# Kernel tuning notes

Hardware: AMD Instinct MI355X
Metric: run time of the kernel (lower is better)

Reference implementation:

```python
import jax, jax.numpy as jnp
import numpy as np

N, C, E, S = 16384, 128, 262144, 10
AVG_NUM_NEIGHBORS = 16.0
INV_SQRT3 = 1.0 / np.sqrt(3.0)


def setup_inputs() -> dict:
    key = jax.random.key(0)
    ks = jax.random.split(key, 15)
    return dict(
        node_specie=jax.random.randint(ks[0], (N,), 0, S),
        node_feats=jax.random.normal(ks[1], (N, C, 4), jnp.float32),   # irreps 0e+1o per channel
        edge_attrs=jax.random.normal(ks[2], (E, 4), jnp.float32),      # Y: 0e+1o
        edge_feats=jax.random.normal(ks[3], (E, 8), jnp.float32),      # radial scalars
        senders=jax.random.randint(ks[4], (E,), 0, N),
        receivers=jax.random.randint(ks[5], (E,), 0, N),
        W_sc0=jax.random.normal(ks[6], (S, C, C), jnp.float32),
        W_sc1=jax.random.normal(ks[7], (S, C, C), jnp.float32),
        W_pre0=jax.random.normal(ks[8], (C, C), jnp.float32),
        W_pre1=jax.random.normal(ks[9], (C, C), jnp.float32),
        W_mlp1=jax.random.normal(ks[10], (8, 64), jnp.float32),
        W_mlp2=jax.random.normal(ks[11], (64, 64), jnp.float32),
        W_mlp3=jax.random.normal(ks[12], (64, 4), jnp.float32),
        W_post0=jax.random.normal(ks[13], (C, 2, C), jnp.float32),
        W_post1=jax.random.normal(ks[14], (C, 2, C), jnp.float32),
    )


def reference(node_specie, node_feats, edge_attrs, edge_feats, senders, receivers,
              W_sc0, W_sc1, W_pre0, W_pre1, W_mlp1, W_mlp2, W_mlp3, W_post0, W_post1):
    inv_c = 1.0 / np.sqrt(C)
    s_in = node_feats[..., 0]      # [N,C] 0e
    v_in = node_feats[..., 1:4]    # [N,C,3] 1o

    # linear_sc: per-species equivariant linear (0e+1o -> hidden 0e+1o)
    sc_s = jnp.einsum('nc,ncd->nd', s_in, W_sc0[node_specie]) * inv_c
    sc_v = jnp.einsum('nci,ncd->ndi', v_in, W_sc1[node_specie]) * inv_c
    sc = jnp.concatenate([sc_s[..., None], sc_v], axis=-1)  # [N,C,4]

    # linear_premp: channel-mixing equivariant linear (same irreps)
    s = (s_in @ W_pre0) * inv_c                              # [N,C]
    v = jnp.einsum('nci,cd->ndi', v_in, W_pre1) * inv_c      # [N,C,3]

    # MessagePassingConvolution (channel axis kept instead of hk.vmap)
    se_s = s[senders]              # [E,C]
    se_v = v[senders]              # [E,C,3]
    a = edge_attrs[:, 1:4]         # drop 0e part of Y -> 1o
    dot = jnp.einsum('eci,ei->ec', se_v, a) * INV_SQRT3      # 1o x 1o -> 0e
    sva = se_s[..., None] * a[:, None, :]                    # 0e x 1o -> 1o

    # radial MLP -> one mixing scalar per irrep (num_irreps = 4), shared across channels
    h = jax.nn.silu((edge_feats @ W_mlp1) * (1.0 / np.sqrt(8.0)))
    h = jax.nn.silu((h @ W_mlp2) * 0.125)
    mix = (h @ W_mlp3) * 0.125                               # [E,4]

    # messages irreps 2x0e+2x1o: [s, dot | v, s*a], each block scaled by its mix scalar
    msg = jnp.concatenate([
        se_s[..., None] * mix[:, None, 0:1],
        dot[..., None] * mix[:, None, 1:2],
        se_v * mix[:, None, 2:3],
        sva * mix[:, None, 3:4],
    ], axis=-1)                                              # [E,C,8]

    agg = jnp.zeros((N, C, 8), msg.dtype).at[receivers].add(msg) / AVG_NUM_NEIGHBORS

    # linear_postmp: (2x0e+2x1o, C channels) -> (0e+1o, C channels)
    inv2c = 1.0 / np.sqrt(2 * C)
    o_s = jnp.einsum('ncm,cmd->nd', agg[..., :2], W_post0) * inv2c
    o_v = jnp.einsum('ncmi,cmd->ndi', agg[..., 2:].reshape(N, C, 2, 3), W_post1) * inv2c
    node_out = jnp.concatenate([o_s[..., None], o_v], axis=-1)  # [N,C,4]
    return node_out, sc
```

## Files before the change

### kernel.cpp

```cpp
#include <hip/hip_runtime.h>
#include <hip/hip_bf16.h>

#define N_NODES 16384
#define C_DIM   128
#define E_EDGES 262144
#define S_SPEC  10
#define CHUNK   256
#define GNODES  32
#define NSLICE  8
#define PROWS   16544
#define PTILES  1034

__device__ __constant__ const float INV_C  = 0.08838834764831845f;
__device__ __constant__ const float INV_2C = 0.0625f;
#define F_INV_SQRT3 0.5773502691896258f
#define F_INV_SQRT8 0.35355339059327373f
#define F_INV_AVG   0.0625f

typedef __attribute__((ext_vector_type(8))) short bf16x8;
typedef __attribute__((ext_vector_type(4))) float f32x4;

__device__ __forceinline__ float silu(float x) {
    return x / (1.0f + __expf(-x));
}

__device__ __forceinline__ unsigned short f2bf(float x) {
    __hip_bfloat16 h = __float2bfloat16(x);
    return *reinterpret_cast<unsigned short*>(&h);
}

__device__ __forceinline__ unsigned int pack2bf(float lo, float hi) {
    return (unsigned int)f2bf(lo) | ((unsigned int)f2bf(hi) << 16);
}

__device__ __forceinline__ float bf2f(unsigned int u16) {
    return __uint_as_float(u16 << 16);
}

__global__ __launch_bounds__(256) void init_kernel(
    int* __restrict__ counts, int* __restrict__ scnt,
    int* __restrict__ prow_map, int* __restrict__ tile_spec)
{
    const int idx = blockIdx.x * 256 + threadIdx.x;
    if (idx < N_NODES) counts[idx] = 0;
    if (idx < S_SPEC)  scnt[idx] = 0;
    if (idx < PROWS)   prow_map[idx] = -1;
    if (idx < PTILES)  tile_spec[idx] = 0;
}

__global__ __launch_bounds__(256) void hist_kernel(
    const int* __restrict__ receivers, int* __restrict__ cnt,
    const int* __restrict__ specie, int* __restrict__ scnt)
{
    __shared__ int h[S_SPEC];
    const int t = threadIdx.x;
    const bool doSpec = blockIdx.x < (N_NODES / 256);
    if (doSpec) {
        if (t < S_SPEC) h[t] = 0;
        __syncthreads();
        atomicAdd(&h[specie[blockIdx.x * 256 + t]], 1);
    }
    const int e = blockIdx.x * 256 + t;
    atomicAdd(&cnt[receivers[e]], 1);
    if (doSpec) {
        __syncthreads();
        if (t < S_SPEC) atomicAdd(&scnt[t], h[t]);
    }
}

__global__ __launch_bounds__(256) void scan_kernel(
    const int* __restrict__ cnt, int* __restrict__ start,
    int* __restrict__ cursor,
    const int* __restrict__ scnt, int* __restrict__ poff,
    int* __restrict__ scur)
{
    __shared__ int sums[256];
    const int t = threadIdx.x;
    if (t == 0) {
        int pa = 0;
        for (int i = 0; i < S_SPEC; ++i) {
            poff[i] = pa;
            scur[i] = 0;
            pa += ((scnt[i] + 15) >> 4) << 4;
        }
    }
    int s = 0;
    for (int i = 0; i < 64; ++i) s += cnt[t * 64 + i];
    sums[t] = s;
    __syncthreads();
    if (t == 0) {
        int a = 0;
        for (int i = 0; i < 256; ++i) { int v = sums[i]; sums[i] = a; a += v; }
    }
    __syncthreads();
    int a = sums[t];
    for (int i = 0; i < 64; ++i) {
        int v = cnt[t * 64 + i];
        start[t * 64 + i] = a;
        cursor[t * 64 + i] = a;
        a += v;
    }
    if (t == 255) start[N_NODES] = a;
}

__global__ __launch_bounds__(256) void scatter_place_kernel(
    const int* __restrict__ receivers, int* __restrict__ cursor,
    int* __restrict__ perm,
    const int* __restrict__ specie, const int* __restrict__ poff,
    int* __restrict__ scur,
    int* __restrict__ prow_map, int* __restrict__ tile_spec)
{
    const int t = threadIdx.x;
    const int e = blockIdx.x * 256 + t;
    const int pos = atomicAdd(&cursor[receivers[e]], 1);
    perm[pos] = e;

    if (blockIdx.x < (N_NODES / 256)) {
        __shared__ int h[S_SPEC];
        __shared__ int bbase[S_SPEC];
        if (t < S_SPEC) h[t] = 0;
        __syncthreads();
        const int n = blockIdx.x * 256 + t;
        const int s = specie[n];
        const int lrank = atomicAdd(&h[s], 1);
        __syncthreads();
        if (t < S_SPEC && h[t] > 0) bbase[t] = atomicAdd(&scur[t], h[t]);
        __syncthreads();
        const int p = poff[s] + bbase[s] + lrank;
        prow_map[p] = n;
        tile_spec[p >> 4] = s;
    }
}

__global__ __launch_bounds__(256) void prep_kernel(
    const int* __restrict__ prow_map, const float* __restrict__ node_feats,
    ushort* __restrict__ As, ushort* __restrict__ Av0,
    ushort* __restrict__ Av1, ushort* __restrict__ Av2,
    const float* __restrict__ Wsc0, const float* __restrict__ Wsc1,
    ushort* __restrict__ Wsc0t, ushort* __restrict__ Wsc1t,
    const float* __restrict__ Wpre0, const float* __restrict__ Wpre1,
    ushort* __restrict__ Wpre0t, ushort* __restrict__ Wpre1t,
    const float* __restrict__ Wp0, const float* __restrict__ Wp1,
    ushort* __restrict__ Bt0, ushort* __restrict__ Bt1,
    const float* __restrict__ Wm1, const float* __restrict__ Wm2,
    const float* __restrict__ Wm3,
    ushort* __restrict__ W1t, ushort* __restrict__ W2t,
    ushort* __restrict__ W3t)
{
    const int idx = blockIdx.x * 256 + threadIdx.x;
    {
        const int p = idx >> 7, c = idx & 127;
        const int nid = prow_map[p];
        float4 f = {0.0f, 0.0f, 0.0f, 0.0f};
        if (nid >= 0) f = ((const float4*)node_feats)[nid * C_DIM + c];
        As [idx] = f2bf(f.x);
        Av0[idx] = f2bf(f.y);
        Av1[idx] = f2bf(f.z);
        Av2[idx] = f2bf(f.w);
    }
    if (idx < S_SPEC * 128 * 128) {
        const int s = idx >> 14, d = (idx >> 7) & 127, k = idx & 127;
        Wsc0t[idx] = f2bf(Wsc0[s * 16384 + k * 128 + d] * INV_C);
        Wsc1t[idx] = f2bf(Wsc1[s * 16384 + k * 128 + d] * INV_C);
    }
    if (idx < 16384) {
        const int d = idx >> 7, k = idx & 127;
        Wpre0t[idx] = f2bf(Wpre0[k * 128 + d] * INV_C);
        Wpre1t[idx] = f2bf(Wpre1[k * 128 + d] * INV_C);
    }
    if (idx < 32768) {
        const int k = idx >> 7, d = idx & 127;
        Bt0[d * 256 + k] = f2bf(Wp0[idx] * INV_2C);
        Bt1[d * 256 + k] = f2bf(Wp1[idx] * INV_2C);
    }
    if (idx < 4096) {
        if (idx < 2048) {
            const int hh = idx >> 5, k = idx & 31;
            W1t[idx] = (k < 8) ? f2bf(Wm1[k * 64 + hh] * F_INV_SQRT8) : (ushort)0;
        }
        {
            const int c = idx >> 6, k = idx & 63;
            W2t[idx] = f2bf(Wm2[k * 64 + c] * 0.125f);
        }
        if (idx < 1024) {
            const int m = idx >> 6, k = idx & 63;
            W3t[idx] = (m < 4) ? f2bf(Wm3[k * 4 + m] * 0.125f) : (ushort)0;
        }
    }
}

__global__ __launch_bounds__(512) void node_gemm_kernel(
    const int* __restrict__ prow_map,
    const int* __restrict__ tile_spec,
    const ushort* __restrict__ As,
    const ushort* __restrict__ Av0,
    const ushort* __restrict__ Av1,
    const ushort* __restrict__ Av2,
    const ushort* __restrict__ Wsc0t,
    const ushort* __restrict__ Wsc1t,
    const ushort* __restrict__ Wpre0t,
    const ushort* __restrict__ Wpre1t,
    float* __restrict__ out_sc,
    ushort4* __restrict__ sv_bf)
{
    const int l  = threadIdx.x & 63;
    const int w  = threadIdx.x >> 6;
    const int d0 = w * 16;
    const int lr = l & 15;
    const int lg = l >> 4;

    bf16x8 bp0[4], bp1[4];
#pragma unroll
    for (int ks = 0; ks < 4; ++ks) {
        bp0[ks] = *reinterpret_cast<const bf16x8*>(
            Wpre0t + (d0 + lr) * 128 + ks * 32 + lg * 8);
        bp1[ks] = *reinterpret_cast<const bf16x8*>(
            Wpre1t + (d0 + lr) * 128 + ks * 32 + lg * 8);
    }

    const int tile = blockIdx.x;
    const int sp   = tile_spec[tile];
    const int r0   = tile * 16;

    const ushort* as  = As  + (size_t)(r0 + lr) * 128 + lg * 8;
    const ushort* av0 = Av0 + (size_t)(r0 + lr) * 128 + lg * 8;
    const ushort* av1 = Av1 + (size_t)(r0 + lr) * 128 + lg * 8;
    const ushort* av2 = Av2 + (size_t)(r0 + lr) * 128 + lg * 8;
    const ushort* ws0 = Wsc0t + (size_t)sp * 16384 + (d0 + lr) * 128 + lg * 8;
    const ushort* ws1 = Wsc1t + (size_t)sp * 16384 + (d0 + lr) * 128 + lg * 8;

    const f32x4 zero = {0.0f, 0.0f, 0.0f, 0.0f};
    f32x4 aS0 = zero, aS1 = zero, aS2 = zero, aS3 = zero;
    f32x4 aP0 = zero, aP1 = zero, aP2 = zero, aP3 = zero;

#pragma unroll
    for (int ks = 0; ks < 4; ++ks) {
        const bf16x8 a_s  = *reinterpret_cast<const bf16x8*>(as  + ks * 32);
        const bf16x8 a_v0 = *reinterpret_cast<const bf16x8*>(av0 + ks * 32);
        const bf16x8 a_v1 = *reinterpret_cast<const bf16x8*>(av1 + ks * 32);
        const bf16x8 a_v2 = *reinterpret_cast<const bf16x8*>(av2 + ks * 32);
        const bf16x8 bs0  = *reinterpret_cast<const bf16x8*>(ws0 + ks * 32);
        const bf16x8 bs1  = *reinterpret_cast<const bf16x8*>(ws1 + ks * 32);
        aS0 = __builtin_amdgcn_mfma_f32_16x16x32_bf16(a_s,  bs0, aS0, 0, 0, 0);
        aS1 = __builtin_amdgcn_mfma_f32_16x16x32_bf16(a_v0, bs1, aS1, 0, 0, 0);
        aS2 = __builtin_amdgcn_mfma_f32_16x16x32_bf16(a_v1, bs1, aS2, 0, 0, 0);
        aS3 = __builtin_amdgcn_mfma_f32_16x16x32_bf16(a_v2, bs1, aS3, 0, 0, 0);
        aP0 = __builtin_amdgcn_mfma_f32_16x16x32_bf16(a_s,  bp0[ks], aP0, 0, 0, 0);
        aP1 = __builtin_amdgcn_mfma_f32_16x16x32_bf16(a_v0, bp1[ks], aP1, 0, 0, 0);
        aP2 = __builtin_amdgcn_mfma_f32_16x16x32_bf16(a_v1, bp1[ks], aP2, 0, 0, 0);
        aP3 = __builtin_amdgcn_mfma_f32_16x16x32_bf16(a_v2, bp1[ks], aP3, 0, 0, 0);
    }

#pragma unroll
    for (int r = 0; r < 4; ++r) {
        const int row = r0 + lg * 4 + r;
        const int nid = prow_map[row];
        if (nid >= 0) {
            float4 o = {aS0[r], aS1[r], aS2[r], aS3[r]};
            ((float4*)out_sc)[(size_t)nid * C_DIM + (d0 + lr)] = o;
            ushort4 pv = {f2bf(aP0[r]), f2bf(aP1[r]), f2bf(aP2[r]), f2bf(aP3[r])};
            sv_bf[(size_t)nid * C_DIM + (d0 + lr)] = pv;
        }
    }
}

__global__ __launch_bounds__(256) void edge_mlp_mfma_kernel(
    const float* __restrict__ edge_feats,
    const float* __restrict__ edge_attrs,
    const ushort* __restrict__ W1t,
    const ushort* __restrict__ W2t,
    const ushort* __restrict__ W3t,
    uint4* __restrict__ coefbf)
{
    __shared__ ushort h_lds[4][16][72];

    const int w  = threadIdx.x >> 6;
    const int l  = threadIdx.x & 63;
    const int lr = l & 15;
    const int lg = l >> 4;

    bf16x8 a1[4];
#pragma unroll
    for (int mt = 0; mt < 4; ++mt)
        a1[mt] = *reinterpret_cast<const bf16x8*>(
            W1t + (mt * 16 + lr) * 32 + lg * 8);
    bf16x8 a2[4][2];
#pragma unroll
    for (int mt = 0; mt < 4; ++mt)
#pragma unroll
        for (int ks = 0; ks < 2; ++ks)
            a2[mt][ks] = *reinterpret_cast<const bf16x8*>(
                W2t + (mt * 16 + lr) * 64 + ks * 32 + lg * 8);
    bf16x8 a3[2];
#pragma unroll
    for (int ks = 0; ks < 2; ++ks)
        a3[ks] = *reinterpret_cast<const bf16x8*>(
            W3t + lr * 64 + ks * 32 + lg * 8);

    const int tile = blockIdx.x * 4 + w;
    const int e0   = tile * 16;
    const f32x4 zero = {0.0f, 0.0f, 0.0f, 0.0f};

    bf16x8 b1 = {0, 0, 0, 0, 0, 0, 0, 0};
    if (lg == 0) {
        const float4 q0 = *(const float4*)(edge_feats + (size_t)(e0 + lr) * 8);
        const float4 q1 = *(const float4*)(edge_feats + (size_t)(e0 + lr) * 8 + 4);
        b1[0] = (short)f2bf(q0.x); b1[1] = (short)f2bf(q0.y);
        b1[2] = (short)f2bf(q0.z); b1[3] = (short)f2bf(q0.w);
        b1[4] = (short)f2bf(q1.x); b1[5] = (short)f2bf(q1.y);
        b1[6] = (short)f2bf(q1.z); b1[7] = (short)f2bf(q1.w);
    }

    f32x4 d1[4];
#pragma unroll
    for (int mt = 0; mt < 4; ++mt)
        d1[mt] = __builtin_amdgcn_mfma_f32_16x16x32_bf16(a1[mt], b1, zero, 0, 0, 0);

#pragma unroll
    for (int mt = 0; mt < 4; ++mt) {
        uint2 p;
        p.x = pack2bf(silu(d1[mt][0]), silu(d1[mt][1]));
        p.y = pack2bf(silu(d1[mt][2]), silu(d1[mt][3]));
        *reinterpret_cast<uint2*>(&h_lds[w][lr][mt * 16 + lg * 4]) = p;
    }
    __syncthreads();

    bf16x8 b2[2];
#pragma unroll
    for (int ks = 0; ks < 2; ++ks)
        b2[ks] = *reinterpret_cast<const bf16x8*>(
            &h_lds[w][lr][ks * 32 + lg * 8]);

    f32x4 d2[4];
#pragma unroll
    for (int mt = 0; mt < 4; ++mt) {
        d2[mt] = __builtin_amdgcn_mfma_f32_16x16x32_bf16(a2[mt][0], b2[0], zero, 0, 0, 0);
        d2[mt] = __builtin_amdgcn_mfma_f32_16x16x32_bf16(a2[mt][1], b2[1], d2[mt], 0, 0, 0);
    }

#pragma unroll
    for (int mt = 0; mt < 4; ++mt) {
        uint2 p;
        p.x = pack2bf(silu(d2[mt][0]), silu(d2[mt][1]));
        p.y = pack2bf(silu(d2[mt][2]), silu(d2[mt][3]));
        *reinterpret_cast<uint2*>(&h_lds[w][lr][mt * 16 + lg * 4]) = p;
    }
    __syncthreads();

    bf16x8 b3[2];
#pragma unroll
    for (int ks = 0; ks < 2; ++ks)
        b3[ks] = *reinterpret_cast<const bf16x8*>(
            &h_lds[w][lr][ks * 32 + lg * 8]);

    f32x4 d3;
    d3 = __builtin_amdgcn_mfma_f32_16x16x32_bf16(a3[0], b3[0], zero, 0, 0, 0);
    d3 = __builtin_amdgcn_mfma_f32_16x16x32_bf16(a3[1], b3[1], d3, 0, 0, 0);

    if (lg == 0) {
        const int e = e0 + lr;
        const float4 a = *(const float4*)(edge_attrs + (size_t)e * 4);
        const float mx0 = d3[0], mx1 = d3[1], mx2 = d3[2], mx3 = d3[3];
        uint4 cv;
        cv.x = pack2bf(mx0,                      mx1 * a.y * F_INV_SQRT3);
        cv.y = pack2bf(mx1 * a.z * F_INV_SQRT3,  mx1 * a.w * F_INV_SQRT3);
        cv.z = pack2bf(mx2,                      mx3 * a.y);
        cv.w = pack2bf(mx3 * a.z,                mx3 * a.w);
        coefbf[e] = cv;
    }
}

__global__ __launch_bounds__(256) void agg_kernel(
    const int* __restrict__ start,
    const int* __restrict__ perm,
    const int* __restrict__ senders,
    const uint4* __restrict__ coefbf,
    const uint4* __restrict__ sv16,
    unsigned int* __restrict__ A_s,
    unsigned int* __restrict__ A_v)
{
    __shared__ int   se_lds[CHUNK];
    __shared__ float sc_lds[CHUNK][8];

    const int slice = blockIdx.x & (NSLICE - 1);
    const int n0    = (blockIdx.x >> 3) * GNODES;
    const int t     = threadIdx.x;
    const int g     = t & 7;
    const int ns    = t >> 3;
    const int n     = n0 + ns;

    const int beg = start[n];
    const int end = start[n + 1];
    const int blk_beg = start[n0];
    const int blk_end = start[n0 + GNODES];

    float acc0[8] = {};
    float acc1[8] = {};

    for (int cb = blk_beg; cb < blk_end; cb += CHUNK) {
        const int cn = min(CHUNK, blk_end - cb);
        __syncthreads();
        for (int j = t; j < cn; j += 256) {
            const int e = perm[cb + j];
            se_lds[j] = senders[e];
            const uint4 cv = coefbf[e];
            float* kf = sc_lds[j];
            kf[0] = bf2f(cv.x & 0xffff); kf[1] = bf2f(cv.x >> 16);
            kf[2] = bf2f(cv.y & 0xffff); kf[3] = bf2f(cv.y >> 16);
            kf[4] = bf2f(cv.z & 0xffff); kf[5] = bf2f(cv.z >> 16);
            kf[6] = bf2f(cv.w & 0xffff); kf[7] = bf2f(cv.w >> 16);
        }
        __syncthreads();

        const int lo = max(beg, cb);
        const int hi = min(end, cb + cn);
        for (int idx = lo; idx < hi; ++idx) {
            const int j = idx - cb;
            const int snd = se_lds[j];
            const float* kf = sc_lds[j];
            const uint4 q = sv16[(size_t)snd * 64 + slice * 8 + g];

            const float x0 = bf2f(q.x & 0xffff), y0 = bf2f(q.x >> 16);
            const float z0 = bf2f(q.y & 0xffff), w0 = bf2f(q.y >> 16);
            const float x1 = bf2f(q.z & 0xffff), y1 = bf2f(q.z >> 16);
            const float z1 = bf2f(q.w & 0xffff), w1 = bf2f(q.w >> 16);

            acc0[0] += x0 * kf[0];
            acc0[1] += y0 * kf[1] + z0 * kf[2] + w0 * kf[3];
            acc0[2] += y0 * kf[4];
            acc0[3] += z0 * kf[4];
            acc0[4] += w0 * kf[4];
            acc0[5] += x0 * kf[5];
            acc0[6] += x0 * kf[6];
            acc0[7] += x0 * kf[7];

            acc1[0] += x1 * kf[0];
            acc1[1] += y1 * kf[1] + z1 * kf[2] + w1 * kf[3];
            acc1[2] += y1 * kf[4];
            acc1[3] += z1 * kf[4];
            acc1[4] += w1 * kf[4];
            acc1[5] += x1 * kf[5];
            acc1[6] += x1 * kf[6];
            acc1[7] += x1 * kf[7];
        }
    }

    const int chp = slice * 8 + g;
    uint2 vs;
    vs.x = pack2bf(acc0[0] * F_INV_AVG, acc0[1] * F_INV_AVG);
    vs.y = pack2bf(acc1[0] * F_INV_AVG, acc1[1] * F_INV_AVG);
    ((uint2*)A_s)[(size_t)n * 64 + chp] = vs;

    uint2 v0;
    v0.x = pack2bf(acc0[2] * F_INV_AVG, acc0[5] * F_INV_AVG);
    v0.y = pack2bf(acc1[2] * F_INV_AVG, acc1[5] * F_INV_AVG);
    ((uint2*)A_v)[((size_t)n * 3 + 0) * 64 + chp] = v0;

    uint2 v1;
    v1.x = pack2bf(acc0[3] * F_INV_AVG, acc0[6] * F_INV_AVG);
    v1.y = pack2bf(acc1[3] * F_INV_AVG, acc1[6] * F_INV_AVG);
    ((uint2*)A_v)[((size_t)n * 3 + 1) * 64 + chp] = v1;

    uint2 v2;
    v2.x = pack2bf(acc0[4] * F_INV_AVG, acc0[7] * F_INV_AVG);
    v2.y = pack2bf(acc1[4] * F_INV_AVG, acc1[7] * F_INV_AVG);
    ((uint2*)A_v)[((size_t)n * 3 + 2) * 64 + chp] = v2;
}

__global__ __launch_bounds__(512) void post_gemm_kernel(
    const ushort* __restrict__ A_s,
    const ushort* __restrict__ A_v,
    const ushort* __restrict__ Bt0,
    const ushort* __restrict__ Bt1,
    float* __restrict__ out)
{
    const int l  = threadIdx.x & 63;
    const int w  = threadIdx.x >> 6;
    const int d0 = w * 16;
    const int lr = l & 15;
    const int lg = l >> 4;

    const bool isS = blockIdx.x < 512;
    const ushort* A  = isS ? A_s : A_v;
    const ushort* Bt = isS ? Bt0 : Bt1;
    const int ntiles  = isS ? (N_NODES / 16) : (3 * N_NODES / 16);
    const int b0      = isS ? blockIdx.x : blockIdx.x - 512;
    const int gstride = isS ? 512 : 1024;

    bf16x8 bfrag[8];
#pragma unroll
    for (int ks = 0; ks < 8; ++ks) {
        bfrag[ks] = *reinterpret_cast<const bf16x8*>(
            Bt + (size_t)(d0 + lr) * 256 + ks * 32 + lg * 8);
    }

    for (int tile = b0; tile < ntiles; tile += gstride) {
        const int r0 = tile * 16;
        f32x4 acc = {0.0f, 0.0f, 0.0f, 0.0f};
        const ushort* ap = A + (size_t)(r0 + lr) * 256 + lg * 8;
#pragma unroll
        for (int ks = 0; ks < 8; ++ks) {
            bf16x8 a = *reinterpret_cast<const bf16x8*>(ap + ks * 32);
            acc = __builtin_amdgcn_mfma_f32_16x16x32_bf16(a, bfrag[ks], acc,
                                                          0, 0, 0);
        }
#pragma unroll
        for (int r = 0; r < 4; ++r) {
            const int row = r0 + lg * 4 + r;
            int n, comp;
            if (isS) { n = row; comp = 0; }
            else { n = row / 3; comp = 1 + (row - n * 3); }
            out[(size_t)n * 512 + (d0 + lr) * 4 + comp] = acc[r];
        }
    }
}

extern "C" void kernel_launch(void* const* d_in, const int* in_sizes, int n_in,
                              void* d_out, int out_size, void* d_ws, size_t ws_size,
                              hipStream_t stream)
{
    const int*   specie     = (const int*)d_in[0];
    const float* node_feats = (const float*)d_in[1];
    const float* edge_attrs = (const float*)d_in[2];
    const float* edge_feats = (const float*)d_in[3];
    const int*   senders    = (const int*)d_in[4];
    const int*   receivers  = (const int*)d_in[5];
    const float* Wsc0  = (const float*)d_in[6];
    const float* Wsc1  = (const float*)d_in[7];
    const float* Wpre0 = (const float*)d_in[8];
    const float* Wpre1 = (const float*)d_in[9];
    const float* Wm1   = (const float*)d_in[10];
    const float* Wm2   = (const float*)d_in[11];
    const float* Wm3   = (const float*)d_in[12];
    const float* Wp0   = (const float*)d_in[13];
    const float* Wp1   = (const float*)d_in[14];

    float* out_node = (float*)d_out;
    float* out_sc   = out_node + (size_t)N_NODES * C_DIM * 4;

    char* ws = (char*)d_ws;
    ushort4*      sv_bf = (ushort4*)ws;
    unsigned int* A_s   = (unsigned int*)(ws + (size_t)16 * 1024 * 1024);
    unsigned int* A_v   = A_s + (size_t)N_NODES * 128;
    uint4*        coefbf= (uint4*)(A_v + (size_t)3 * N_NODES * 128);
    ushort*       Asin  = (ushort*)(coefbf + (size_t)E_EDGES);
    ushort*       Av0in = Asin  + (size_t)PROWS * 128;
    ushort*       Av1in = Av0in + (size_t)PROWS * 128;
    ushort*       Av2in = Av1in + (size_t)PROWS * 128;
    ushort*       Bt0   = Av2in + (size_t)PROWS * 128;
    ushort*       Bt1   = Bt0 + 256 * 128;
    ushort*       Wsc0t = Bt1 + 256 * 128;
    ushort*       Wsc1t = Wsc0t + S_SPEC * 128 * 128;
    ushort*       Wpre0t = Wsc1t + S_SPEC * 128 * 128;
    ushort*       Wpre1t = Wpre0t + 128 * 128;
    ushort*       W1t   = Wpre1t + 128 * 128;
    ushort*       W2t   = W1t + 64 * 32;
    ushort*       W3t   = W2t + 64 * 64;
    int* counts    = (int*)(W3t + 16 * 64);
    int* start     = counts + N_NODES;
    int* cursor    = start + (N_NODES + 1);
    int* perm      = cursor + N_NODES;
    int* scnt      = perm + E_EDGES;
    int* poff      = scnt + S_SPEC;
    int* scur      = poff + S_SPEC;
    int* prow_map  = scur + S_SPEC;
    int* tile_spec = prow_map + PROWS;

    init_kernel<<<(PROWS + 255) / 256, 256, 0, stream>>>(
        counts, scnt, prow_map, tile_spec);

    hist_kernel<<<E_EDGES / 256, 256, 0, stream>>>(
        receivers, counts, specie, scnt);

    scan_kernel<<<1, 256, 0, stream>>>(counts, start, cursor, scnt, poff, scur);

    scatter_place_kernel<<<E_EDGES / 256, 256, 0, stream>>>(
        receivers, cursor, perm, specie, poff, scur, prow_map, tile_spec);

    prep_kernel<<<PROWS * 128 / 256, 256, 0, stream>>>(
        prow_map, node_feats, Asin, Av0in, Av1in, Av2in,
        Wsc0, Wsc1, Wsc0t, Wsc1t, Wpre0, Wpre1, Wpre0t, Wpre1t,
        Wp0, Wp1, Bt0, Bt1, Wm1, Wm2, Wm3, W1t, W2t, W3t);

    node_gemm_kernel<<<PTILES, 512, 0, stream>>>(
        prow_map, tile_spec, Asin, Av0in, Av1in, Av2in,
        Wsc0t, Wsc1t, Wpre0t, Wpre1t, out_sc, sv_bf);

    edge_mlp_mfma_kernel<<<E_EDGES / 64, 256, 0, stream>>>(
        edge_feats, edge_attrs, W1t, W2t, W3t, coefbf);

    agg_kernel<<<NSLICE * (N_NODES / GNODES), 256, 0, stream>>>(
        start, perm, senders, coefbf, (const uint4*)sv_bf, A_s, A_v);

    post_gemm_kernel<<<1536, 512, 0, stream>>>(
        (const ushort*)A_s, (const ushort*)A_v, Bt0, Bt1, out_node);
}
```

Baseline: 260.1 us.

## Restructure aggregation: thread per channel, 8 nodes per block, unroll edge pairs

The aggregation kernel now gives each block 8 receiver nodes, with each thread owning one channel and accumulating for 4 nodes, instead of slicing channels across 8 blocks per 32-node group. This stops each block's edge chunk (perm, senders, coefficients) from being reloaded and reconverted once per slice, and removes the bf16 shift-and-mask work through a pair of helpers. The inner edge loop is also unrolled by two so that two gathers are in flight at once. In exchange, each thread's gather shrinks to 8 bytes, each thread carries 32 accumulators, and imbalance across the 4 nodes in a thread can leave lanes idle.

```diff
diff --git a/kernel.cpp b/kernel.cpp
--- a/kernel.cpp
+++ b/kernel.cpp
@@ -6,8 +6,6 @@
 #define E_EDGES 262144
 #define S_SPEC  10
 #define CHUNK   256
-#define GNODES  32
-#define NSLICE  8
 #define PROWS   16544
 #define PTILES  1034
 
@@ -34,7 +32,11 @@
 }
 
 __device__ __forceinline__ float bf2f(unsigned int u16) {
-    return __uint_as_float(u16 << 16);
+    return __uint_as_float((u16 & 0xffffu) << 16);
+}
+
+__device__ __forceinline__ float bf2f_hi(unsigned int u) {
+    return __uint_as_float(u & 0xffff0000u);
 }
 
 __global__ __launch_bounds__(256) void init_kernel(
@@ -375,27 +377,29 @@
     const int* __restrict__ perm,
     const int* __restrict__ senders,
     const uint4* __restrict__ coefbf,
-    const uint4* __restrict__ sv16,
+    const ushort4* __restrict__ sv_bf,
     unsigned int* __restrict__ A_s,
     unsigned int* __restrict__ A_v)
 {
     __shared__ int   se_lds[CHUNK];
     __shared__ float sc_lds[CHUNK][8];
 
-    const int slice = blockIdx.x & (NSLICE - 1);
-    const int n0    = (blockIdx.x >> 3) * GNODES;
-    const int t     = threadIdx.x;
-    const int g     = t & 7;
-    const int ns    = t >> 3;
-    const int n     = n0 + ns;
-
-    const int beg = start[n];
-    const int end = start[n + 1];
+    const int n0   = blockIdx.x * 8;
+    const int t    = threadIdx.x;
+    const int c    = t & 127;
+    const int half = t >> 7;
+
+    int nbeg[4], nend[4];
+#pragma unroll
+    for (int k = 0; k < 4; ++k) {
+        nbeg[k] = start[n0 + half * 4 + k];
+        nend[k] = start[n0 + half * 4 + k + 1];
+    }
+
     const int blk_beg = start[n0];
-    const int blk_end = start[n0 + GNODES];
-
-    float acc0[8] = {};
-    float acc1[8] = {};
+    const int blk_end = start[n0 + 8];
+
+    float acc[4][8] = {};
 
     for (int cb = blk_beg; cb < blk_end; cb += CHUNK) {
         const int cn = min(CHUNK, blk_end - cb);
@@ -404,67 +408,78 @@
             const int e = perm[cb + j];
             se_lds[j] = senders[e];
             const uint4 cv = coefbf[e];
-            float* kf = sc_lds[j];
-            kf[0] = bf2f(cv.x & 0xffff); kf[1] = bf2f(cv.x >> 16);
-            kf[2] = bf2f(cv.y & 0xffff); kf[3] = bf2f(cv.y >> 16);
-            kf[4] = bf2f(cv.z & 0xffff); kf[5] = bf2f(cv.z >> 16);
-            kf[6] = bf2f(cv.w & 0xffff); kf[7] = bf2f(cv.w >> 16);
+            float4 lo = {bf2f(cv.x), bf2f_hi(cv.x), bf2f(cv.y), bf2f_hi(cv.y)};
+            float4 hi = {bf2f(cv.z), bf2f_hi(cv.z), bf2f(cv.w), bf2f_hi(cv.w)};
+            ((float4*)sc_lds[j])[0] = lo;
+            ((float4*)sc_lds[j])[1] = hi;
         }
         __syncthreads();
 
-        const int lo = max(beg, cb);
-        const int hi = min(end, cb + cn);
-        for (int idx = lo; idx < hi; ++idx) {
-            const int j = idx - cb;
-            const int snd = se_lds[j];
-            const float* kf = sc_lds[j];
-            const uint4 q = sv16[(size_t)snd * 64 + slice * 8 + g];
-
-            const float x0 = bf2f(q.x & 0xffff), y0 = bf2f(q.x >> 16);
-            const float z0 = bf2f(q.y & 0xffff), w0 = bf2f(q.y >> 16);
-            const float x1 = bf2f(q.z & 0xffff), y1 = bf2f(q.z >> 16);
-            const float z1 = bf2f(q.w & 0xffff), w1 = bf2f(q.w >> 16);
-
-            acc0[0] += x0 * kf[0];
-            acc0[1] += y0 * kf[1] + z0 * kf[2] + w0 * kf[3];
-            acc0[2] += y0 * kf[4];
-            acc0[3] += z0 * kf[4];
-            acc0[4] += w0 * kf[4];
-            acc0[5] += x0 * kf[5];
-            acc0[6] += x0 * kf[6];
-            acc0[7] += x0 * kf[7];
-
-            acc1[0] += x1 * kf[0];
-            acc1[1] += y1 * kf[1] + z1 * kf[2] + w1 * kf[3];
-            acc1[2] += y1 * kf[4];
-            acc1[3] += z1 * kf[4];
-            acc1[4] += w1 * kf[4];
-            acc1[5] += x1 * kf[5];
-            acc1[6] += x1 * kf[6];
-            acc1[7] += x1 * kf[7];
-        }
-    }
-
-    const int chp = slice * 8 + g;
-    uint2 vs;
-    vs.x = pack2bf(acc0[0] * F_INV_AVG, acc0[1] * F_INV_AVG);
-    vs.y = pack2bf(acc1[0] * F_INV_AVG, acc1[1] * F_INV_AVG);
-    ((uint2*)A_s)[(size_t)n * 64 + chp] = vs;
-
-    uint2 v0;
-    v0.x = pack2bf(acc0[2] * F_INV_AVG, acc0[5] * F_INV_AVG);
-    v0.y = pack2bf(acc1[2] * F_INV_AVG, acc1[5] * F_INV_AVG);
-    ((uint2*)A_v)[((size_t)n * 3 + 0) * 64 + chp] = v0;
-
-    uint2 v1;
-    v1.x = pack2bf(acc0[3] * F_INV_AVG, acc0[6] * F_INV_AVG);
-    v1.y = pack2bf(acc1[3] * F_INV_AVG, acc1[6] * F_INV_AVG);
-    ((uint2*)A_v)[((size_t)n * 3 + 1) * 64 + chp] = v1;
-
-    uint2 v2;
-    v2.x = pack2bf(acc0[4] * F_INV_AVG, acc0[7] * F_INV_AVG);
-    v2.y = pack2bf(acc1[4] * F_INV_AVG, acc1[7] * F_INV_AVG);
-    ((uint2*)A_v)[((size_t)n * 3 + 2) * 64 + chp] = v2;
+#pragma unroll
+        for (int k = 0; k < 4; ++k) {
+            const int lo = max(nbeg[k], cb);
+            const int hi = min(nend[k], cb + cn);
+            int idx = lo;
+            for (; idx + 2 <= hi; idx += 2) {
+                const int j0 = idx - cb, j1 = j0 + 1;
+                const int snd0 = se_lds[j0];
+                const int snd1 = se_lds[j1];
+                const ushort4 u0 = sv_bf[(size_t)snd0 * C_DIM + c];
+                const ushort4 u1 = sv_bf[(size_t)snd1 * C_DIM + c];
+                const float* kf0 = sc_lds[j0];
+                const float* kf1 = sc_lds[j1];
+                const float x0 = bf2f(u0.x), y0 = bf2f(u0.y),
+                            z0 = bf2f(u0.z), w0 = bf2f(u0.w);
+                const float x1 = bf2f(u1.x), y1 = bf2f(u1.y),
+                            z1 = bf2f(u1.z), w1 = bf2f(u1.w);
+                acc[k][0] += x0 * kf0[0];
+                acc[k][1] += y0 * kf0[1] + z0 * kf0[2] + w0 * kf0[3];
+                acc[k][2] += y0 * kf0[4];
+                acc[k][3] += z0 * kf0[4];
+                acc[k][4] += w0 * kf0[4];
+                acc[k][5] += x0 * kf0[5];
+                acc[k][6] += x0 * kf0[6];
+                acc[k][7] += x0 * kf0[7];
+                acc[k][0] += x1 * kf1[0];
+                acc[k][1] += y1 * kf1[1] + z1 * kf1[2] + w1 * kf1[3];
+                acc[k][2] += y1 * kf1[4];
+                acc[k][3] += z1 * kf1[4];
+                acc[k][4] += w1 * kf1[4];
+                acc[k][5] += x1 * kf1[5];
+                acc[k][6] += x1 * kf1[6];
+                acc[k][7] += x1 * kf1[7];
+            }
+            if (idx < hi) {
+                const int j = idx - cb;
+                const int snd = se_lds[j];
+                const ushort4 u = sv_bf[(size_t)snd * C_DIM + c];
+                const float* kf = sc_lds[j];
+                const float x = bf2f(u.x), y = bf2f(u.y),
+                            z = bf2f(u.z), w = bf2f(u.w);
+                acc[k][0] += x * kf[0];
+                acc[k][1] += y * kf[1] + z * kf[2] + w * kf[3];
+                acc[k][2] += y * kf[4];
+                acc[k][3] += z * kf[4];
+                acc[k][4] += w * kf[4];
+                acc[k][5] += x * kf[5];
+                acc[k][6] += x * kf[6];
+                acc[k][7] += x * kf[7];
+            }
+        }
+    }
+
+#pragma unroll
+    for (int k = 0; k < 4; ++k) {
+        const int n = n0 + half * 4 + k;
+        A_s[(size_t)n * 128 + c] =
+            pack2bf(acc[k][0] * F_INV_AVG, acc[k][1] * F_INV_AVG);
+        A_v[((size_t)n * 3 + 0) * 128 + c] =
+            pack2bf(acc[k][2] * F_INV_AVG, acc[k][5] * F_INV_AVG);
+        A_v[((size_t)n * 3 + 1) * 128 + c] =
+            pack2bf(acc[k][3] * F_INV_AVG, acc[k][6] * F_INV_AVG);
+        A_v[((size_t)n * 3 + 2) * 128 + c] =
+            pack2bf(acc[k][4] * F_INV_AVG, acc[k][7] * F_INV_AVG);
+    }
 }
 
 __global__ __launch_bounds__(512) void post_gemm_kernel(
@@ -589,8 +604,8 @@
     edge_mlp_mfma_kernel<<<E_EDGES / 64, 256, 0, stream>>>(
         edge_feats, edge_attrs, W1t, W2t, W3t, coefbf);
 
-    agg_kernel<<<NSLICE * (N_NODES / GNODES), 256, 0, stream>>>(
-        start, perm, senders, coefbf, (const uint4*)sv_bf, A_s, A_v);
+    agg_kernel<<<N_NODES / 8, 256, 0, stream>>>(
+        start, perm, senders, coefbf, sv_bf, A_s, A_v);
 
     post_gemm_kernel<<<1536, 512, 0, stream>>>(
         (const ushort*)A_s, (const ushort*)A_v, Bt0, Bt1, out_node);
```

Result: faster. 228.0 us (-12.3%).
